# Optimization experiments

Hardware: AMD Instinct MI355X
Metric: run time of the kernel (lower is better)

Reference implementation:

```python
import jax, jax.numpy as jnp
import numpy as np
import math

EMBED_DIM = 512
NHEAD = 8
HEAD_DIM = EMBED_DIM // NHEAD
B, L = 32, 512
EPS = 1e-5


def layer_norm(x, gamma, beta):
    mu = jnp.mean(x, axis=-1, keepdims=True)
    var = jnp.var(x, axis=-1, keepdims=True)
    return (x - mu) * jax.lax.rsqrt(var + EPS) * gamma + beta


def setup_inputs() -> dict:
    key = jax.random.key(0)
    ks = jax.random.split(key, 16)
    D = EMBED_DIM
    s = 1.0 / math.sqrt(D)
    return {
        "x": jax.random.normal(ks[0], (B, L, D), dtype=jnp.float32),
        "inter": jax.random.normal(ks[1], (B, L, L, 4), dtype=jnp.float32),
        "qkv_w": jax.random.normal(ks[2], (D, 3 * D), dtype=jnp.float32) * s,
        "qkv_b": jnp.zeros((3 * D,), dtype=jnp.float32),
        "out_w": jax.random.normal(ks[3], (D, D), dtype=jnp.float32) * s,
        "out_b": jnp.zeros((D,), dtype=jnp.float32),
        "norm1_g": jnp.ones((D,), dtype=jnp.float32),
        "norm1_b": jnp.zeros((D,), dtype=jnp.float32),
        "norm2_g": jnp.ones((D,), dtype=jnp.float32),
        "norm2_b": jnp.zeros((D,), dtype=jnp.float32),
        "inter_w": jax.random.normal(ks[4], (4, NHEAD), dtype=jnp.float32) * 0.5,
        "ffn_w1": jax.random.normal(ks[5], (D, 4 * D), dtype=jnp.float32) * s,
        "ffn_b1": jnp.zeros((4 * D,), dtype=jnp.float32),
        "ffn_w2": jax.random.normal(ks[6], (4 * D, D), dtype=jnp.float32) * (1.0 / math.sqrt(4 * D)),
        "ffn_b2": jnp.zeros((D,), dtype=jnp.float32),
    }


def reference(x, inter, qkv_w, qkv_b, out_w, out_b, norm1_g, norm1_b,
              norm2_g, norm2_b, inter_w, ffn_w1, ffn_b1, ffn_w2, ffn_b2):
    Bb, Ll, D = x.shape
    residual = x
    h = layer_norm(x, norm1_g, norm1_b)
    qkv = (h @ qkv_w + qkv_b).reshape(Bb, Ll, 3, NHEAD, HEAD_DIM)
    qkv = jnp.transpose(qkv, (2, 0, 3, 1, 4))  # (3, B, H, L, hd)
    q, k, v = qkv[0], qkv[1], qkv[2]
    scale = math.sqrt(HEAD_DIM)
    scores = jnp.einsum("bhqd,bhkd->bhqk", q, k) / scale
    # pairwise interaction bias: (B,L,L,4) @ (4,H) -> (B,H,L,L)
    bias = jnp.einsum("bqkf,fh->bhqk", inter, inter_w)
    attn = jax.nn.softmax(scores + bias, axis=-1)
    # dropout p=0 in eval mode
    out = jnp.einsum("bhqk,bhkd->bhqd", attn, v)
    out = jnp.transpose(out, (0, 2, 1, 3)).reshape(Bb, Ll, D)
    x = residual + out @ out_w + out_b
    h2 = layer_norm(x, norm2_g, norm2_b)
    ffn = jax.nn.gelu(h2 @ ffn_w1 + ffn_b1, approximate=False) @ ffn_w2 + ffn_b2
    return x + ffn
```

## Files before the change

kernel.cpp:

```cpp
#include <hip/hip_runtime.h>
#include <math.h>

#define BB 32
#define LL 512
#define DD 512
#define NH 8
#define HD 64

typedef __attribute__((ext_vector_type(8))) short bf16x8;
typedef __attribute__((ext_vector_type(4))) float f32x4;

__device__ __forceinline__ unsigned short f2bf(float x) {
    union { float f; unsigned u; } v; v.f = x;
    unsigned r = v.u + 0x7fffu + ((v.u >> 16) & 1u);
    return (unsigned short)(r >> 16);
}

__device__ __forceinline__ float warp_sum(float v) {
    #pragma unroll
    for (int o = 32; o > 0; o >>= 1) v += __shfl_down(v, o);
    return v;
}

__global__ void ln_kernel(const float* __restrict__ X, const float* __restrict__ g,
                          const float* __restrict__ b, unsigned short* __restrict__ Y) {
    __shared__ float red[8];
    const size_t base = (size_t)blockIdx.x * DD;
    const int t = threadIdx.x;
    float x0 = X[base + t], x1 = X[base + t + 256];
    float s = warp_sum(x0 + x1);
    float q = warp_sum(x0 * x0 + x1 * x1);
    if ((t & 63) == 0) { red[t >> 6] = s; red[4 + (t >> 6)] = q; }
    __syncthreads();
    float S = red[0] + red[1] + red[2] + red[3];
    float Q = red[4] + red[5] + red[6] + red[7];
    float mu  = S * (1.0f / 512.0f);
    float var = Q * (1.0f / 512.0f) - mu * mu;
    float r = rsqrtf(var + 1e-5f);
    Y[base + t]       = f2bf((x0 - mu) * r * g[t] + b[t]);
    Y[base + t + 256] = f2bf((x1 - mu) * r * g[t + 256] + b[t + 256]);
}

__global__ void transpose_bf16(const float* __restrict__ W, unsigned short* __restrict__ WT,
                               int K, int N) {
    __shared__ float t[32][33];
    const int n0 = blockIdx.x * 32, k0 = blockIdx.y * 32;
    const int tx = threadIdx.x & 31, ty = threadIdx.x >> 5;
    #pragma unroll
    for (int r = 0; r < 32; r += 8)
        t[ty + r][tx] = W[(size_t)(k0 + ty + r) * N + n0 + tx];
    __syncthreads();
    #pragma unroll
    for (int r = 0; r < 32; r += 8)
        WT[(size_t)(n0 + ty + r) * K + k0 + tx] = f2bf(t[tx][ty + r]);
}

template <int ACT, int RES, int OM>
__global__ __launch_bounds__(256)
void gemm_mfma(const unsigned short* __restrict__ A, const unsigned short* __restrict__ BT,
               const float* __restrict__ bias, const float* __restrict__ res,
               void* __restrict__ Cv, unsigned short* __restrict__ kfrag,
               unsigned short* __restrict__ vfrag, int M, int N, int K) {
    __shared__ unsigned short As[128 * 64];
    __shared__ unsigned short Bs[128 * 64];
    const int tid = threadIdx.x;
    const int wave = tid >> 6, lane = tid & 63;
    const int wm = (wave >> 1) * 64, wn = (wave & 1) * 64;
    const int bm = blockIdx.y * 128, bn = blockIdx.x * 128;

    f32x4 acc[4][4] = {};

    for (int k0 = 0; k0 < K; k0 += 64) {
        __syncthreads();
        #pragma unroll
        for (int it = 0; it < 4; ++it) {
            const int s = it * 256 + tid;
            const int row = s >> 3, pch = s & 7;
            const int lch = pch ^ (row & 7);
            const unsigned short* ga = A + (size_t)(bm + row) * K + k0 + lch * 8;
            __builtin_amdgcn_global_load_lds(
                (const __attribute__((address_space(1))) void*)ga,
                (__attribute__((address_space(3))) void*)(As + s * 8), 16, 0, 0);
            const unsigned short* gb = BT + (size_t)(bn + row) * K + k0 + lch * 8;
            __builtin_amdgcn_global_load_lds(
                (const __attribute__((address_space(1))) void*)gb,
                (__attribute__((address_space(3))) void*)(Bs + s * 8), 16, 0, 0);
        }
        __syncthreads();
        #pragma unroll
        for (int ks = 0; ks < 2; ++ks) {
            bf16x8 af[4], bfr[4];
            #pragma unroll
            for (int i = 0; i < 4; ++i) {
                const int row = wm + i * 16 + (lane & 15);
                const int pch = (ks * 4 + (lane >> 4)) ^ (row & 7);
                af[i] = *(const bf16x8*)(As + row * 64 + pch * 8);
            }
            #pragma unroll
            for (int j = 0; j < 4; ++j) {
                const int row = wn + j * 16 + (lane & 15);
                const int pch = (ks * 4 + (lane >> 4)) ^ (row & 7);
                bfr[j] = *(const bf16x8*)(Bs + row * 64 + pch * 8);
            }
            #pragma unroll
            for (int i = 0; i < 4; ++i)
                #pragma unroll
                for (int j = 0; j < 4; ++j)
                    acc[i][j] = __builtin_amdgcn_mfma_f32_16x16x32_bf16(
                        af[i], bfr[j], acc[i][j], 0, 0, 0);
        }
    }

    const int cl = lane & 15, rq = (lane >> 4) * 4;
    #pragma unroll
    for (int j = 0; j < 4; ++j) {
        const int col = bn + wn + j * 16 + cl;
        const float bv = bias[col];
        #pragma unroll
        for (int i = 0; i < 4; ++i) {
            const int r0 = bm + wm + i * 16 + rq;
            #pragma unroll
            for (int r = 0; r < 4; ++r) {
                float v = acc[i][j][r] + bv;
                if (ACT == 1) v = 0.5f * v * (1.0f + erff(v * 0.70710678118654752f));
                if (RES) v += res[(size_t)(r0 + r) * N + col];
                if (OM == 0) {
                    ((float*)Cv)[(size_t)(r0 + r) * N + col] = v;
                } else if (OM == 1) {
                    ((unsigned short*)Cv)[(size_t)(r0 + r) * N + col] = f2bf(v);
                } else {
                    const int row = r0 + r;
                    const int b = row >> 9, kpos = row & 511;
                    if (col < 512) {
                        ((unsigned short*)Cv)[(size_t)row * 512 + col] = f2bf(v);
                    } else if (col < 1024) {
                        const int h = (col - 512) >> 6, dd = (col - 512) & 63;
                        const int kt = kpos >> 6, jj = (kpos >> 4) & 3, lo2 = kpos & 15;
                        const int kk = dd >> 5, hi2 = (dd >> 3) & 3, e = dd & 7;
                        kfrag[((((size_t)(b * NH + h) * 8 + kt) * 2 + kk) * 4 + jj) * 512
                              + (hi2 * 16 + lo2) * 8 + e] = f2bf(v);
                    } else {
                        const int h = (col - 1024) >> 6, dd = (col - 1024) & 63;
                        const int kt = kpos >> 6, kk = (kpos >> 5) & 1, hi2 = (kpos >> 3) & 3, e = kpos & 7;
                        const int jj = dd >> 4, lo2 = dd & 15;
                        vfrag[((((size_t)(b * NH + h) * 8 + kt) * 2 + kk) * 4 + jj) * 512
                              + (hi2 * 16 + lo2) * 8 + e] = f2bf(v);
                    }
                }
            }
        }
    }
}

__global__ __launch_bounds__(512)
void flash_kernel(const unsigned short* __restrict__ qbuf,
                  const unsigned short* __restrict__ kfrag,
                  const unsigned short* __restrict__ vfrag,
                  const float* __restrict__ inter,
                  const float* __restrict__ iw,
                  unsigned short* __restrict__ O) {
    __shared__ float it0[16 * 260];
    __shared__ float it1[16 * 260];
    __shared__ unsigned short plds[8][16 * 72];
    const int qg = blockIdx.x, b = blockIdx.y;
    const int tid = threadIdx.x, wave = tid >> 6, lane = tid & 63;
    const int h = wave;
    const int lo = lane & 15, hi = lane >> 4;

    const float iw0 = iw[h], iw1 = iw[8 + h], iw2 = iw[16 + h], iw3 = iw[24 + h];
    const float* interb = inter + (size_t)b * 512 * 512 * 4;
    unsigned short* pw = &plds[wave][0];

    const unsigned short* qp = qbuf + ((size_t)(b * 512 + qg * 16 + lo)) * 512 + h * 64 + hi * 8;
    const bf16x8 qf0 = *(const bf16x8*)(qp);
    const bf16x8 qf1 = *(const bf16x8*)(qp + 32);

    const int srow = wave * 2;
    const float* src0 = interb + ((size_t)(qg * 16 + srow) * 512) * 4 + lane * 4;
    const float* src1 = interb + ((size_t)(qg * 16 + srow + 1) * 512) * 4 + lane * 4;

    f32x4 o[4] = {};
    float m = -1e30f, lsum = 0.0f;

    {
        const float4 a0 = *(const float4*)src0;
        const float4 a1 = *(const float4*)src1;
        *(float4*)(it0 + srow * 260 + lane * 4) = a0;
        *(float4*)(it0 + (srow + 1) * 260 + lane * 4) = a1;
    }

    auto iter = [&](int kt, const float* __restrict__ rd, float* __restrict__ st) {
        const size_t fb = (((size_t)((b * NH + h) * 8 + kt)) * 2) * 4 * 512;
        __syncthreads();
        bf16x8 kf0[4], kf1[4];
        #pragma unroll
        for (int j = 0; j < 4; ++j)
            kf0[j] = *(const bf16x8*)(kfrag + fb + (size_t)j * 512 + lane * 8);
        #pragma unroll
        for (int j = 0; j < 4; ++j)
            kf1[j] = *(const bf16x8*)(kfrag + fb + (size_t)(4 + j) * 512 + lane * 8);
        __builtin_amdgcn_sched_barrier(0);
        f32x4 s[4] = {};
        __builtin_amdgcn_s_setprio(1);
        #pragma unroll
        for (int j = 0; j < 4; ++j)
            s[j] = __builtin_amdgcn_mfma_f32_16x16x32_bf16(kf0[j], qf0, s[j], 0, 0, 0);
        #pragma unroll
        for (int j = 0; j < 4; ++j)
            s[j] = __builtin_amdgcn_mfma_f32_16x16x32_bf16(kf1[j], qf1, s[j], 0, 0, 0);
        __builtin_amdgcn_s_setprio(0);
        const float4* brow = (const float4*)(rd + lo * 260);
        #pragma unroll
        for (int j = 0; j < 4; ++j)
            #pragma unroll
            for (int r = 0; r < 4; ++r) {
                const float4 f = brow[j * 16 + hi * 4 + r];
                s[j][r] = s[j][r] * 0.125f + f.x * iw0 + f.y * iw1 + f.z * iw2 + f.w * iw3;
            }
        bf16x8 vf0[4], vf1[4];
        #pragma unroll
        for (int j = 0; j < 4; ++j)
            vf0[j] = *(const bf16x8*)(vfrag + fb + (size_t)j * 512 + lane * 8);
        #pragma unroll
        for (int j = 0; j < 4; ++j)
            vf1[j] = *(const bf16x8*)(vfrag + fb + (size_t)(4 + j) * 512 + lane * 8);
        __builtin_amdgcn_sched_barrier(0);
        float4 sn0, sn1;
        if (kt < 7) {
            sn0 = *(const float4*)(src0 + (kt + 1) * 256);
            sn1 = *(const float4*)(src1 + (kt + 1) * 256);
        }
        __builtin_amdgcn_sched_barrier(0);
        float t0 = fmaxf(fmaxf(s[0][0], s[0][1]), fmaxf(s[0][2], s[0][3]));
        float t1 = fmaxf(fmaxf(s[1][0], s[1][1]), fmaxf(s[1][2], s[1][3]));
        float t2 = fmaxf(fmaxf(s[2][0], s[2][1]), fmaxf(s[2][2], s[2][3]));
        float t3 = fmaxf(fmaxf(s[3][0], s[3][1]), fmaxf(s[3][2], s[3][3]));
        float mx = fmaxf(fmaxf(t0, t1), fmaxf(t2, t3));
        mx = fmaxf(mx, __shfl_xor(mx, 16));
        mx = fmaxf(mx, __shfl_xor(mx, 32));
        const float mn = fmaxf(m, mx);
        const float al = __expf(m - mn);
        m = mn;
        #pragma unroll
        for (int j = 0; j < 4; ++j)
            #pragma unroll
            for (int r = 0; r < 4; ++r)
                s[j][r] = __expf(s[j][r] - mn);
        float u0 = (s[0][0] + s[0][1]) + (s[0][2] + s[0][3]);
        float u1 = (s[1][0] + s[1][1]) + (s[1][2] + s[1][3]);
        float u2 = (s[2][0] + s[2][1]) + (s[2][2] + s[2][3]);
        float u3 = (s[3][0] + s[3][1]) + (s[3][2] + s[3][3]);
        float ts = (u0 + u1) + (u2 + u3);
        ts += __shfl_xor(ts, 16);
        ts += __shfl_xor(ts, 32);
        lsum = lsum * al + ts;
        const float aR0 = __shfl(al, hi * 4 + 0);
        const float aR1 = __shfl(al, hi * 4 + 1);
        const float aR2 = __shfl(al, hi * 4 + 2);
        const float aR3 = __shfl(al, hi * 4 + 3);
        #pragma unroll
        for (int j2 = 0; j2 < 4; ++j2) {
            o[j2][0] *= aR0; o[j2][1] *= aR1; o[j2][2] *= aR2; o[j2][3] *= aR3;
        }
        uint2* pq = (uint2*)(pw + lo * 72);
        #pragma unroll
        for (int j = 0; j < 4; ++j) {
            uint2 d;
            d.x = (unsigned)f2bf(s[j][0]) | ((unsigned)f2bf(s[j][1]) << 16);
            d.y = (unsigned)f2bf(s[j][2]) | ((unsigned)f2bf(s[j][3]) << 16);
            pq[j * 4 + hi] = d;
        }
        __builtin_amdgcn_s_setprio(1);
        #pragma unroll
        for (int kk = 0; kk < 2; ++kk) {
            const bf16x8 pf = *(const bf16x8*)(pw + lo * 72 + kk * 32 + hi * 8);
            #pragma unroll
            for (int j2 = 0; j2 < 4; ++j2)
                o[j2] = __builtin_amdgcn_mfma_f32_16x16x32_bf16(
                    pf, kk ? vf1[j2] : vf0[j2], o[j2], 0, 0, 0);
        }
        __builtin_amdgcn_s_setprio(0);
        if (kt < 7) {
            *(float4*)(st + srow * 260 + lane * 4) = sn0;
            *(float4*)(st + (srow + 1) * 260 + lane * 4) = sn1;
        }
    };

    for (int kt2 = 0; kt2 < 4; ++kt2) {
        iter(kt2 * 2, it0, it1);
        iter(kt2 * 2 + 1, it1, it0);
    }

    const float iR0 = 1.0f / __shfl(lsum, hi * 4 + 0);
    const float iR1 = 1.0f / __shfl(lsum, hi * 4 + 1);
    const float iR2 = 1.0f / __shfl(lsum, hi * 4 + 2);
    const float iR3 = 1.0f / __shfl(lsum, hi * 4 + 3);
    const int qC0 = qg * 16 + hi * 4;
    #pragma unroll
    for (int j2 = 0; j2 < 4; ++j2) {
        O[(size_t)(b * 512 + qC0 + 0) * 512 + h * 64 + j2 * 16 + lo] = f2bf(o[j2][0] * iR0);
        O[(size_t)(b * 512 + qC0 + 1) * 512 + h * 64 + j2 * 16 + lo] = f2bf(o[j2][1] * iR1);
        O[(size_t)(b * 512 + qC0 + 2) * 512 + h * 64 + j2 * 16 + lo] = f2bf(o[j2][2] * iR2);
        O[(size_t)(b * 512 + qC0 + 3) * 512 + h * 64 + j2 * 16 + lo] = f2bf(o[j2][3] * iR3);
    }
}

extern "C" void kernel_launch(void* const* d_in, const int* in_sizes, int n_in,
                              void* d_out, int out_size, void* d_ws, size_t ws_size,
                              hipStream_t stream) {
    const float* x     = (const float*)d_in[0];
    const float* inter = (const float*)d_in[1];
    const float* qkv_w = (const float*)d_in[2];
    const float* qkv_b = (const float*)d_in[3];
    const float* out_w = (const float*)d_in[4];
    const float* out_b = (const float*)d_in[5];
    const float* n1g   = (const float*)d_in[6];
    const float* n1b   = (const float*)d_in[7];
    const float* n2g   = (const float*)d_in[8];
    const float* n2b   = (const float*)d_in[9];
    const float* iw    = (const float*)d_in[10];
    const float* fw1   = (const float*)d_in[11];
    const float* fb1   = (const float*)d_in[12];
    const float* fw2   = (const float*)d_in[13];
    const float* fb2   = (const float*)d_in[14];
    float* out = (float*)d_out;

    if (ws_size < 190840832ull) return;
    char* ws = (char*)d_ws;
    unsigned short* qbuf    = (unsigned short*)(ws);
    unsigned short* kfrag   = (unsigned short*)(ws + 16777216ull);
    unsigned short* vfrag   = (unsigned short*)(ws + 33554432ull);
    unsigned short* attnout = (unsigned short*)(ws + 50331648ull);
    float*          x2      = (float*)(ws + 67108864ull);
    unsigned short* h_bf    = (unsigned short*)(ws + 100663296ull);
    unsigned short* ffnmid  = (unsigned short*)(ws + 117440512ull);
    unsigned short* qkv_wT  = (unsigned short*)(ws + 184549376ull);
    unsigned short* out_wT  = (unsigned short*)(ws + 186122240ull);
    unsigned short* fw1T    = (unsigned short*)(ws + 186646528ull);
    unsigned short* fw2T    = (unsigned short*)(ws + 188743680ull);

    const int M = BB * LL;

    transpose_bf16<<<dim3(1536 / 32, 512 / 32), 256, 0, stream>>>(qkv_w, qkv_wT, 512, 1536);
    transpose_bf16<<<dim3(512 / 32, 512 / 32), 256, 0, stream>>>(out_w, out_wT, 512, 512);
    transpose_bf16<<<dim3(2048 / 32, 512 / 32), 256, 0, stream>>>(fw1, fw1T, 512, 2048);
    transpose_bf16<<<dim3(512 / 32, 2048 / 32), 256, 0, stream>>>(fw2, fw2T, 2048, 512);
    ln_kernel<<<M, 256, 0, stream>>>(x, n1g, n1b, h_bf);
    gemm_mfma<0, 0, 2><<<dim3(1536 / 128, M / 128), 256, 0, stream>>>(
        h_bf, qkv_wT, qkv_b, nullptr, qbuf, kfrag, vfrag, M, 1536, 512);
    flash_kernel<<<dim3(LL / 16, BB), 512, 0, stream>>>(qbuf, kfrag, vfrag, inter, iw, attnout);
    gemm_mfma<0, 1, 0><<<dim3(512 / 128, M / 128), 256, 0, stream>>>(
        attnout, out_wT, out_b, x, x2, nullptr, nullptr, M, 512, 512);
    ln_kernel<<<M, 256, 0, stream>>>(x2, n2g, n2b, h_bf);
    gemm_mfma<1, 0, 1><<<dim3(2048 / 128, M / 128), 256, 0, stream>>>(
        h_bf, fw1T, fb1, nullptr, ffnmid, nullptr, nullptr, M, 2048, 512);
    gemm_mfma<0, 1, 0><<<dim3(512 / 128, M / 128), 256, 0, stream>>>(
        ffnmid, fw2T, fb2, x2, out, nullptr, nullptr, M, 512, 2048);
}
```

Measured before the change: 546.6 us.

## Read interaction bias directly from global per wave, drop LDS double buffer

Removes the shared-memory double-buffered staging of the pairwise interaction tile and the per-iteration block barrier. Each wave now loads its own bias values straight from global memory in MFMA-output layout, inside a simple non-unrolled loop. K/V fragment loads switch to nontemporal loads. This drops LDS traffic and synchronisation but makes all eight head-waves re-read the same bias data from cache, raising L1/L2 traffic on the largest input.

```diff
diff --git a/kernel.cpp b/kernel.cpp
--- a/kernel.cpp
+++ b/kernel.cpp
@@ -159,8 +159,6 @@
                   const float* __restrict__ inter,
                   const float* __restrict__ iw,
                   unsigned short* __restrict__ O) {
-    __shared__ float it0[16 * 260];
-    __shared__ float it1[16 * 260];
     __shared__ unsigned short plds[8][16 * 72];
     const int qg = blockIdx.x, b = blockIdx.y;
     const int tid = threadIdx.x, wave = tid >> 6, lane = tid & 63;
@@ -168,73 +166,57 @@
     const int lo = lane & 15, hi = lane >> 4;
 
     const float iw0 = iw[h], iw1 = iw[8 + h], iw2 = iw[16 + h], iw3 = iw[24 + h];
-    const float* interb = inter + (size_t)b * 512 * 512 * 4;
     unsigned short* pw = &plds[wave][0];
+
+    const float* bp = inter + (((size_t)b * 512 + qg * 16 + lo) * 512 + hi * 4) * 4;
 
     const unsigned short* qp = qbuf + ((size_t)(b * 512 + qg * 16 + lo)) * 512 + h * 64 + hi * 8;
     const bf16x8 qf0 = *(const bf16x8*)(qp);
     const bf16x8 qf1 = *(const bf16x8*)(qp + 32);
 
-    const int srow = wave * 2;
-    const float* src0 = interb + ((size_t)(qg * 16 + srow) * 512) * 4 + lane * 4;
-    const float* src1 = interb + ((size_t)(qg * 16 + srow + 1) * 512) * 4 + lane * 4;
+    const unsigned short* kfb = kfrag + (size_t)(b * NH + h) * 8 * 4096 + (size_t)lane * 8;
+    const unsigned short* vfb = vfrag + (size_t)(b * NH + h) * 8 * 4096 + (size_t)lane * 8;
 
     f32x4 o[4] = {};
     float m = -1e30f, lsum = 0.0f;
 
-    {
-        const float4 a0 = *(const float4*)src0;
-        const float4 a1 = *(const float4*)src1;
-        *(float4*)(it0 + srow * 260 + lane * 4) = a0;
-        *(float4*)(it0 + (srow + 1) * 260 + lane * 4) = a1;
-    }
-
-    auto iter = [&](int kt, const float* __restrict__ rd, float* __restrict__ st) {
-        const size_t fb = (((size_t)((b * NH + h) * 8 + kt)) * 2) * 4 * 512;
-        __syncthreads();
-        bf16x8 kf0[4], kf1[4];
+    #pragma unroll 1
+    for (int kt = 0; kt < 8; ++kt) {
+        const unsigned short* kp = kfb + kt * 4096;
+        bf16x8 kf[8];
+        #pragma unroll
+        for (int jj = 0; jj < 8; ++jj)
+            kf[jj] = __builtin_nontemporal_load((const bf16x8*)(kp + jj * 512));
+        f32x4 s4[4] = {};
+        __builtin_amdgcn_s_setprio(1);
         #pragma unroll
         for (int j = 0; j < 4; ++j)
-            kf0[j] = *(const bf16x8*)(kfrag + fb + (size_t)j * 512 + lane * 8);
+            s4[j] = __builtin_amdgcn_mfma_f32_16x16x32_bf16(kf[j], qf0, s4[j], 0, 0, 0);
         #pragma unroll
         for (int j = 0; j < 4; ++j)
-            kf1[j] = *(const bf16x8*)(kfrag + fb + (size_t)(4 + j) * 512 + lane * 8);
-        __builtin_amdgcn_sched_barrier(0);
-        f32x4 s[4] = {};
-        __builtin_amdgcn_s_setprio(1);
-        #pragma unroll
-        for (int j = 0; j < 4; ++j)
-            s[j] = __builtin_amdgcn_mfma_f32_16x16x32_bf16(kf0[j], qf0, s[j], 0, 0, 0);
-        #pragma unroll
-        for (int j = 0; j < 4; ++j)
-            s[j] = __builtin_amdgcn_mfma_f32_16x16x32_bf16(kf1[j], qf1, s[j], 0, 0, 0);
+            s4[j] = __builtin_amdgcn_mfma_f32_16x16x32_bf16(kf[4 + j], qf1, s4[j], 0, 0, 0);
         __builtin_amdgcn_s_setprio(0);
-        const float4* brow = (const float4*)(rd + lo * 260);
-        #pragma unroll
-        for (int j = 0; j < 4; ++j)
-            #pragma unroll
-            for (int r = 0; r < 4; ++r) {
-                const float4 f = brow[j * 16 + hi * 4 + r];
-                s[j][r] = s[j][r] * 0.125f + f.x * iw0 + f.y * iw1 + f.z * iw2 + f.w * iw3;
-            }
-        bf16x8 vf0[4], vf1[4];
-        #pragma unroll
-        for (int j = 0; j < 4; ++j)
-            vf0[j] = *(const bf16x8*)(vfrag + fb + (size_t)j * 512 + lane * 8);
-        #pragma unroll
-        for (int j = 0; j < 4; ++j)
-            vf1[j] = *(const bf16x8*)(vfrag + fb + (size_t)(4 + j) * 512 + lane * 8);
-        __builtin_amdgcn_sched_barrier(0);
-        float4 sn0, sn1;
-        if (kt < 7) {
-            sn0 = *(const float4*)(src0 + (kt + 1) * 256);
-            sn1 = *(const float4*)(src1 + (kt + 1) * 256);
-        }
-        __builtin_amdgcn_sched_barrier(0);
-        float t0 = fmaxf(fmaxf(s[0][0], s[0][1]), fmaxf(s[0][2], s[0][3]));
-        float t1 = fmaxf(fmaxf(s[1][0], s[1][1]), fmaxf(s[1][2], s[1][3]));
-        float t2 = fmaxf(fmaxf(s[2][0], s[2][1]), fmaxf(s[2][2], s[2][3]));
-        float t3 = fmaxf(fmaxf(s[3][0], s[3][1]), fmaxf(s[3][2], s[3][3]));
+        const float* bk = bp + (size_t)kt * 256;
+        #pragma unroll
+        for (int j = 0; j < 4; ++j) {
+            const float4 c0 = *(const float4*)(bk + j * 64);
+            const float4 c1 = *(const float4*)(bk + j * 64 + 4);
+            const float4 c2 = *(const float4*)(bk + j * 64 + 8);
+            const float4 c3 = *(const float4*)(bk + j * 64 + 12);
+            s4[j][0] = s4[j][0] * 0.125f + c0.x * iw0 + c0.y * iw1 + c0.z * iw2 + c0.w * iw3;
+            s4[j][1] = s4[j][1] * 0.125f + c1.x * iw0 + c1.y * iw1 + c1.z * iw2 + c1.w * iw3;
+            s4[j][2] = s4[j][2] * 0.125f + c2.x * iw0 + c2.y * iw1 + c2.z * iw2 + c2.w * iw3;
+            s4[j][3] = s4[j][3] * 0.125f + c3.x * iw0 + c3.y * iw1 + c3.z * iw2 + c3.w * iw3;
+        }
+        const unsigned short* vp = vfb + kt * 4096;
+        bf16x8 vf[8];
+        #pragma unroll
+        for (int jj = 0; jj < 8; ++jj)
+            vf[jj] = __builtin_nontemporal_load((const bf16x8*)(vp + jj * 512));
+        float t0 = fmaxf(fmaxf(s4[0][0], s4[0][1]), fmaxf(s4[0][2], s4[0][3]));
+        float t1 = fmaxf(fmaxf(s4[1][0], s4[1][1]), fmaxf(s4[1][2], s4[1][3]));
+        float t2 = fmaxf(fmaxf(s4[2][0], s4[2][1]), fmaxf(s4[2][2], s4[2][3]));
+        float t3 = fmaxf(fmaxf(s4[3][0], s4[3][1]), fmaxf(s4[3][2], s4[3][3]));
         float mx = fmaxf(fmaxf(t0, t1), fmaxf(t2, t3));
         mx = fmaxf(mx, __shfl_xor(mx, 16));
         mx = fmaxf(mx, __shfl_xor(mx, 32));
@@ -245,11 +227,11 @@
         for (int j = 0; j < 4; ++j)
             #pragma unroll
             for (int r = 0; r < 4; ++r)
-                s[j][r] = __expf(s[j][r] - mn);
-        float u0 = (s[0][0] + s[0][1]) + (s[0][2] + s[0][3]);
-        float u1 = (s[1][0] + s[1][1]) + (s[1][2] + s[1][3]);
-        float u2 = (s[2][0] + s[2][1]) + (s[2][2] + s[2][3]);
-        float u3 = (s[3][0] + s[3][1]) + (s[3][2] + s[3][3]);
+                s4[j][r] = __expf(s4[j][r] - mn);
+        float u0 = (s4[0][0] + s4[0][1]) + (s4[0][2] + s4[0][3]);
+        float u1 = (s4[1][0] + s4[1][1]) + (s4[1][2] + s4[1][3]);
+        float u2 = (s4[2][0] + s4[2][1]) + (s4[2][2] + s4[2][3]);
+        float u3 = (s4[3][0] + s4[3][1]) + (s4[3][2] + s4[3][3]);
         float ts = (u0 + u1) + (u2 + u3);
         ts += __shfl_xor(ts, 16);
         ts += __shfl_xor(ts, 32);
@@ -266,8 +248,8 @@
         #pragma unroll
         for (int j = 0; j < 4; ++j) {
             uint2 d;
-            d.x = (unsigned)f2bf(s[j][0]) | ((unsigned)f2bf(s[j][1]) << 16);
-            d.y = (unsigned)f2bf(s[j][2]) | ((unsigned)f2bf(s[j][3]) << 16);
+            d.x = (unsigned)f2bf(s4[j][0]) | ((unsigned)f2bf(s4[j][1]) << 16);
+            d.y = (unsigned)f2bf(s4[j][2]) | ((unsigned)f2bf(s4[j][3]) << 16);
             pq[j * 4 + hi] = d;
         }
         __builtin_amdgcn_s_setprio(1);
@@ -277,18 +259,9 @@
             #pragma unroll
             for (int j2 = 0; j2 < 4; ++j2)
                 o[j2] = __builtin_amdgcn_mfma_f32_16x16x32_bf16(
-                    pf, kk ? vf1[j2] : vf0[j2], o[j2], 0, 0, 0);
+                    pf, vf[kk * 4 + j2], o[j2], 0, 0, 0);
         }
         __builtin_amdgcn_s_setprio(0);
-        if (kt < 7) {
-            *(float4*)(st + srow * 260 + lane * 4) = sn0;
-            *(float4*)(st + (srow + 1) * 260 + lane * 4) = sn1;
-        }
-    };
-
-    for (int kt2 = 0; kt2 < 4; ++kt2) {
-        iter(kt2 * 2, it0, it1);
-        iter(kt2 * 2 + 1, it1, it0);
     }
 
     const float iR0 = 1.0f / __shfl(lsum, hi * 4 + 0);
```

New measurement: 679.0 us. 24.2% more time.
